# Kernel tuning notes

Hardware: AMD Instinct MI355X
Metric: run time of the kernel (lower is better)

The kernel has to match this reference:

```python
import jax, jax.numpy as jnp
import numpy as np

N, M, G = 50000, 400000, 128   # nodes, undirected edges, graphs
FN, FE, L, O = 128, 32, 128, 128
MAX_LV = 3


def setup_inputs() -> dict:
    rng = np.random.default_rng(0)
    key = jax.random.key(0)
    ks = jax.random.split(key, 12)
    # random multigraph without self-loops; directed edges interleaved so that
    # edge 2i = (u->v) and edge 2i+1 = (v->u) (reverse edge = e ^ 1)
    u = rng.integers(0, N, size=M)
    v = (u + 1 + rng.integers(0, N - 1, size=M)) % N
    src = np.empty(2 * M, dtype=np.int32)
    dst = np.empty(2 * M, dtype=np.int32)
    src[0::2], src[1::2] = u, v
    dst[0::2], dst[1::2] = v, u
    graph_ids = np.sort(rng.integers(0, G, size=N)).astype(np.int32)

    def lin(k, fan_in, fan_out):
        return jax.random.normal(k, (fan_in, fan_out), jnp.float32) / np.sqrt(fan_in)

    return {
        "node_feat": jax.random.normal(ks[0], (N, FN), jnp.float32),
        "edge_feat": jax.random.normal(ks[1], (2 * M, FE), jnp.float32),
        "w_n2l_W": lin(ks[2], FN, L), "w_n2l_b": jnp.zeros((L,), jnp.float32),
        "w_e2l_W": lin(ks[3], FE, L), "w_e2l_b": jnp.zeros((L,), jnp.float32),
        "conv_W": lin(ks[4], L, L),   "conv_b": jnp.zeros((L,), jnp.float32),
        "out_W": lin(ks[5], L, O),    "out_b": jnp.zeros((O,), jnp.float32),
        "edge_src": jnp.asarray(src),
        "edge_dst": jnp.asarray(dst),
        "graph_ids": jnp.asarray(graph_ids),
        "num_graphs": G,
    }


def _swap_reverse(msgs):
    # message of the reverse directed edge: pairs are interleaved (2i, 2i+1)
    E, D = msgs.shape
    return msgs.reshape(E // 2, 2, D)[:, ::-1, :].reshape(E, D)


def reference(node_feat, edge_feat, w_n2l_W, w_n2l_b, w_e2l_W, w_e2l_b,
              conv_W, conv_b, out_W, out_b, edge_src, edge_dst, graph_ids,
              num_graphs):
    n_nodes = node_feat.shape[0]
    # n2e_sp @ (W_n node_feat): gather source-node linear features onto edges
    input_node_linear = node_feat @ w_n2l_W + w_n2l_b          # [N, L]
    input_message = input_node_linear[edge_src]                # [E, L]
    input_message = input_message + (edge_feat @ w_e2l_W + w_e2l_b)
    cur = jax.nn.relu(input_message)                           # input_potential
    for _ in range(MAX_LV):
        # e2e_sp @ cur: sum of messages into src node, minus reverse edge
        node_agg = jax.ops.segment_sum(cur, edge_dst, num_segments=n_nodes)
        e2epool = node_agg[edge_src] - _swap_reverse(cur)      # [E, L]
        cur = jax.nn.relu(e2epool @ conv_W + conv_b + input_message)
    # e2n_sp @ cur: sum edge messages into destination nodes
    e2npool = jax.ops.segment_sum(cur, edge_dst, num_segments=n_nodes)
    hidden_msg = jax.nn.relu(e2npool)                          # [N, L]
    reluact = jax.nn.relu(hidden_msg @ out_W + out_b)          # [N, O]
    # subg_sp @ reluact: pool nodes per graph
    y = jax.ops.segment_sum(reluact, graph_ids, num_segments=num_graphs)
    return jax.nn.relu(y)                                      # [G, O]
```

## Files before the change

kernel.cpp:

```cpp
#include <hip/hip_runtime.h>
#include <hip/hip_bf16.h>
#include <stdint.h>

typedef __attribute__((ext_vector_type(8))) short short8;
typedef __attribute__((ext_vector_type(4))) float f32x4;

__device__ __forceinline__ float b2f(ushort u) {
  union { uint32_t i; float f; } v; v.i = ((uint32_t)u) << 16; return v.f;
}
__device__ __forceinline__ ushort f2b(float f) {
  union { float f; uint32_t i; } v; v.f = f;
  uint32_t x = v.i;
  uint32_t r = x + 0x7FFFu + ((x >> 16) & 1u);
  return (ushort)(r >> 16);
}
__device__ __forceinline__ uint pk2(float lo, float hi) {
  return (uint)f2b(lo) | ((uint)f2b(hi) << 16);
}
__device__ __forceinline__ float lo2f(uint v) { return b2f((ushort)(v & 0xFFFFu)); }
__device__ __forceinline__ float hi2f(uint v) { return b2f((ushort)(v >> 16)); }

__device__ __forceinline__ uint4 pkf8(float4 a, float4 b) {
  uint4 o;
  o.x = pk2(a.x, a.y); o.y = pk2(a.z, a.w);
  o.z = pk2(b.x, b.y); o.w = pk2(b.z, b.w);
  return o;
}
__device__ __forceinline__ uint sub2(uint a, uint b) {
  return pk2(lo2f(a) - lo2f(b), hi2f(a) - hi2f(b));
}
__device__ __forceinline__ uint4 sub8(uint4 a, uint4 b) {
  uint4 o; o.x = sub2(a.x,b.x); o.y = sub2(a.y,b.y); o.z = sub2(a.z,b.z); o.w = sub2(a.w,b.w); return o;
}
__device__ __forceinline__ uint relu2(uint v) {
  uint lo = (v & 0x8000u) ? 0u : (v & 0xFFFFu);
  uint hi = (v & 0x80000000u) ? 0u : (v & 0xFFFF0000u);
  return lo | hi;
}
__device__ __forceinline__ uint4 relu8(uint4 v) {
  uint4 o; o.x = relu2(v.x); o.y = relu2(v.y); o.z = relu2(v.z); o.w = relu2(v.w); return o;
}

__global__ void zero_ints(int* __restrict__ p, int n) {
  int i = blockIdx.x * blockDim.x + threadIdx.x;
  if (i < n) p[i] = 0;
}

__global__ void prep_weights(const float* __restrict__ wn, const float* __restrict__ we,
                             const float* __restrict__ cw, const float* __restrict__ ow,
                             const float* __restrict__ cb, const float* __restrict__ be,
                             ushort* __restrict__ wnT, ushort* __restrict__ weT,
                             ushort* __restrict__ cweT, ushort* __restrict__ owT,
                             float* __restrict__ cbe) {
  int i = blockIdx.x * blockDim.x + threadIdx.x;
  if (i < 16384) {
    int n = i >> 7, k = i & 127; wnT[n*128+k] = f2b(wn[k*128+n]);
  } else if (i < 32768) {
    int j = i - 16384; int n = j >> 7, k = j & 127; owT[n*128+k] = f2b(ow[k*128+n]);
  } else if (i < 53248) {
    int j = i - 32768;
    int n = j / 160, k = j % 160;
    cweT[n*160+k] = (k < 128) ? f2b(cw[k*128+n]) : f2b(we[(k-128)*128+n]);
  } else if (i < 57344) {
    int j = i - 53248; int n = j >> 5, k = j & 31; weT[n*32+k] = f2b(we[k*128+n]);
  } else if (i < 57472) {
    int j = i - 57344; cbe[j] = cb[j] + be[j];
  }
}

__global__ void count_dst(const int* __restrict__ dst, int* __restrict__ counts, int E) {
  for (int i = blockIdx.x * blockDim.x + threadIdx.x; i < E; i += gridDim.x * blockDim.x)
    atomicAdd(&counts[dst[i]], 1);
}
__global__ __launch_bounds__(1024) void scan_offsets(
    const int* __restrict__ counts, int* __restrict__ off,
    int* __restrict__ cursor, int N) {
  __shared__ int part[1024];
  int t = threadIdx.x;
  int chunk = (N + 1023) >> 10;
  int lo = t * chunk, hi = min(lo + chunk, N);
  int s = 0;
  for (int i = lo; i < hi; ++i) s += counts[i];
  part[t] = s;
  __syncthreads();
  for (int d = 1; d < 1024; d <<= 1) {
    int v = (t >= d) ? part[t - d] : 0;
    __syncthreads();
    part[t] += v;
    __syncthreads();
  }
  int run = (t > 0) ? part[t - 1] : 0;
  for (int i = lo; i < hi; ++i) {
    off[i] = run; cursor[i] = run; run += counts[i];
  }
  if (t == 1023) off[N] = part[1023];
}
__global__ void fill_csr(const int* __restrict__ dst, int* __restrict__ cursor,
                         int* __restrict__ eids, int E) {
  for (int i = blockIdx.x * blockDim.x + threadIdx.x; i < E; i += gridDim.x * blockDim.x) {
    int p = atomicAdd(&cursor[dst[i]], 1);
    eids[p] = i;
  }
}

__global__ __launch_bounds__(256) void node_linear(
    const float* __restrict__ nf, const ushort* __restrict__ wnT,
    const float* __restrict__ bn, ushort* __restrict__ inl, int N) {
  __shared__ ushort Als[64][136];
  __shared__ ushort Bls[128][136];
  int tid = threadIdx.x;
  int n0 = blockIdx.x * 64;
  {
    int row = tid >> 1, h = tid & 1;
    const uint4* gp = (const uint4*)(wnT + row*128 + h*64);
    uint4* lp = (uint4*)&Bls[row][h*64];
    #pragma unroll
    for (int i = 0; i < 8; ++i) lp[i] = gp[i];
  }
  {
    int r = tid >> 2, q = tid & 3;
    int n = n0 + r;
    uint4* lp = (uint4*)&Als[r][q*32];
    if (n < N) {
      const float4* fp = (const float4*)(nf + (size_t)n*128 + q*32);
      #pragma unroll
      for (int i = 0; i < 4; ++i) lp[i] = pkf8(fp[2*i], fp[2*i+1]);
    } else {
      uint4 z = {0,0,0,0};
      #pragma unroll
      for (int i = 0; i < 4; ++i) lp[i] = z;
    }
  }
  __syncthreads();
  int l = tid & 63, w = tid >> 6, quad = l >> 4, mr = l & 15;
  f32x4 acc[8];
  #pragma unroll
  for (int nt = 0; nt < 8; ++nt) acc[nt] = (f32x4){0.f,0.f,0.f,0.f};
  #pragma unroll
  for (int kk = 0; kk < 4; ++kk) {
    short8 a = *(const short8*)&Als[w*16 + mr][kk*32 + quad*8];
    #pragma unroll
    for (int nt = 0; nt < 8; ++nt) {
      short8 b = *(const short8*)&Bls[nt*16 + mr][kk*32 + quad*8];
      acc[nt] = __builtin_amdgcn_mfma_f32_16x16x32_bf16(a, b, acc[nt], 0, 0, 0);
    }
  }
  #pragma unroll
  for (int nt = 0; nt < 8; ++nt) {
    int col = nt*16 + mr;
    float bias = bn[col];
    #pragma unroll
    for (int rg = 0; rg < 4; ++rg) {
      int n = n0 + w*16 + quad*4 + rg;
      if (n < N) inl[(size_t)n*128 + col] = f2b(acc[nt][rg] + bias);
    }
  }
}

__global__ __launch_bounds__(256) void edge_init(
    const float* __restrict__ ef, const ushort* __restrict__ weT,
    const float* __restrict__ be, const int* __restrict__ esrc,
    const ushort* __restrict__ inl, ushort* __restrict__ cur, int E) {
  __shared__ ushort Als[64][40];
  __shared__ ushort Bls[128][40];
  int tid = threadIdx.x;
  int e0 = blockIdx.x * 64;
  {
    int row = tid >> 1, h = tid & 1;
    const uint4* gp = (const uint4*)(weT + row*32 + h*16);
    uint4* lp = (uint4*)&Bls[row][h*16];
    lp[0] = gp[0]; lp[1] = gp[1];
  }
  {
    int r = tid >> 2, q = tid & 3;
    int e = e0 + r;
    const float4* fp = (const float4*)(ef + (size_t)e*32 + q*8);
    *(uint4*)&Als[r][q*8] = pkf8(fp[0], fp[1]);
  }
  __syncthreads();
  int l = tid & 63, w = tid >> 6, quad = l >> 4, mr = l & 15;
  short8 a = *(const short8*)&Als[w*16 + mr][quad*8];
  f32x4 zero = (f32x4){0.f,0.f,0.f,0.f};
  f32x4 acc[8];
  #pragma unroll
  for (int nt = 0; nt < 8; ++nt) {
    short8 b = *(const short8*)&Bls[nt*16 + mr][quad*8];
    acc[nt] = __builtin_amdgcn_mfma_f32_16x16x32_bf16(a, b, zero, 0, 0, 0);
  }
  int sfour[4];
  #pragma unroll
  for (int rg = 0; rg < 4; ++rg) sfour[rg] = esrc[e0 + w*16 + quad*4 + rg];
  #pragma unroll
  for (int nt = 0; nt < 8; ++nt) {
    int col = nt*16 + mr;
    float bias = be[col];
    #pragma unroll
    for (int rg = 0; rg < 4; ++rg) {
      int e = e0 + w*16 + quad*4 + rg;
      float v = acc[nt][rg] + bias + b2f(inl[(size_t)sfour[rg]*128 + col]);
      cur[(size_t)e*128 + col] = f2b(fmaxf(v, 0.f));
    }
  }
}

__global__ __launch_bounds__(256) void segsum(
    const ushort* __restrict__ cur, const int* __restrict__ off,
    const int* __restrict__ eids, ushort* __restrict__ nagg, int N) {
  int w = threadIdx.x >> 6, l = threadIdx.x & 63;
  int n = blockIdx.x * 4 + w;
  if (n >= N) return;
  int i = off[n], end = off[n + 1];
  float s0 = 0.f, s1 = 0.f;
  for (; i + 4 <= end; i += 4) {
    int ea = eids[i], eb = eids[i + 1], ec = eids[i + 2], ed = eids[i + 3];
    uint va = *(const uint*)(cur + (size_t)ea*128 + 2*l);
    uint vb = *(const uint*)(cur + (size_t)eb*128 + 2*l);
    uint vc = *(const uint*)(cur + (size_t)ec*128 + 2*l);
    uint vd = *(const uint*)(cur + (size_t)ed*128 + 2*l);
    s0 += (lo2f(va) + lo2f(vb)) + (lo2f(vc) + lo2f(vd));
    s1 += (hi2f(va) + hi2f(vb)) + (hi2f(vc) + hi2f(vd));
  }
  for (; i < end; ++i) {
    int ea = eids[i];
    uint va = *(const uint*)(cur + (size_t)ea*128 + 2*l);
    s0 += lo2f(va); s1 += hi2f(va);
  }
  *(uint*)(nagg + (size_t)n*128 + 2*l) = pk2(s0, s1);
}

__global__ __launch_bounds__(256) void conv_step(
    ushort* __restrict__ cur, const ushort* __restrict__ nagg,
    const ushort* __restrict__ inl, const float* __restrict__ ef,
    const ushort* __restrict__ cweT, const float* __restrict__ cbe,
    const int* __restrict__ esrc, int E) {
  __shared__ ushort Als[64][168];
  int tid = threadIdx.x;
  int e0 = blockIdx.x * 64;
  int l = tid & 63, w = tid >> 6, quad = l >> 4, mr = l & 15;

  short8 bfrag[2][5];
  #pragma unroll
  for (int nt = 0; nt < 2; ++nt) {
    const ushort* bp = cweT + (size_t)(w*32 + nt*16 + mr) * 160;
    #pragma unroll
    for (int kk = 0; kk < 5; ++kk)
      bfrag[nt][kk] = *(const short8*)(bp + kk*32 + quad*8);
  }

  {
    int r = tid >> 2, q = tid & 3;
    int e = e0 + r;
    int s = esrc[e];
    const uint4* cp = (const uint4*)(cur + (size_t)(e ^ 1)*128 + q*32);
    const uint4* np = (const uint4*)(nagg + (size_t)s*128 + q*32);
    uint4* lp = (uint4*)&Als[r][q*32];
    #pragma unroll
    for (int i = 0; i < 4; ++i) lp[i] = sub8(np[i], cp[i]);
    const float4* fp = (const float4*)(ef + (size_t)e*32 + q*8);
    *(uint4*)&Als[r][128 + q*8] = pkf8(fp[0], fp[1]);
  }
  __syncthreads();

  #pragma unroll
  for (int m = 0; m < 4; ++m) {
    f32x4 acc0 = (f32x4){0.f,0.f,0.f,0.f};
    f32x4 acc1 = (f32x4){0.f,0.f,0.f,0.f};
    #pragma unroll
    for (int kk = 0; kk < 5; ++kk) {
      short8 a = *(const short8*)&Als[m*16 + mr][kk*32 + quad*8];
      acc0 = __builtin_amdgcn_mfma_f32_16x16x32_bf16(a, bfrag[0][kk], acc0, 0, 0, 0);
      acc1 = __builtin_amdgcn_mfma_f32_16x16x32_bf16(a, bfrag[1][kk], acc1, 0, 0, 0);
    }
    int ebase = e0 + m*16 + quad*4;
    int sfour[4];
    #pragma unroll
    for (int rg = 0; rg < 4; ++rg) sfour[rg] = esrc[ebase + rg];
    int col0 = w*32 + mr, col1 = w*32 + 16 + mr;
    float bias0 = cbe[col0], bias1 = cbe[col1];
    #pragma unroll
    for (int rg = 0; rg < 4; ++rg) {
      float v0 = acc0[rg] + bias0 + b2f(inl[(size_t)sfour[rg]*128 + col0]);
      float v1 = acc1[rg] + bias1 + b2f(inl[(size_t)sfour[rg]*128 + col1]);
      cur[(size_t)(ebase + rg)*128 + col0] = f2b(fmaxf(v0, 0.f));
      cur[(size_t)(ebase + rg)*128 + col1] = f2b(fmaxf(v1, 0.f));
    }
  }
}

__global__ __launch_bounds__(256) void out_linear(
    const ushort* __restrict__ nagg, const ushort* __restrict__ owT,
    const float* __restrict__ ob, ushort* __restrict__ ract, int N) {
  __shared__ ushort Als[64][136];
  __shared__ ushort Bls[128][136];
  int tid = threadIdx.x;
  int n0 = blockIdx.x * 64;
  {
    int row = tid >> 1, h = tid & 1;
    const uint4* gp = (const uint4*)(owT + row*128 + h*64);
    uint4* lp = (uint4*)&Bls[row][h*64];
    #pragma unroll
    for (int i = 0; i < 8; ++i) lp[i] = gp[i];
  }
  {
    int r = tid >> 2, q = tid & 3;
    int n = n0 + r;
    uint4* lp = (uint4*)&Als[r][q*32];
    if (n < N) {
      const uint4* gp = (const uint4*)(nagg + (size_t)n*128 + q*32);
      #pragma unroll
      for (int i = 0; i < 4; ++i) lp[i] = relu8(gp[i]);
    } else {
      uint4 z = {0,0,0,0};
      #pragma unroll
      for (int i = 0; i < 4; ++i) lp[i] = z;
    }
  }
  __syncthreads();
  int l = tid & 63, w = tid >> 6, quad = l >> 4, mr = l & 15;
  f32x4 acc[8];
  #pragma unroll
  for (int nt = 0; nt < 8; ++nt) acc[nt] = (f32x4){0.f,0.f,0.f,0.f};
  #pragma unroll
  for (int kk = 0; kk < 4; ++kk) {
    short8 a = *(const short8*)&Als[w*16 + mr][kk*32 + quad*8];
    #pragma unroll
    for (int nt = 0; nt < 8; ++nt) {
      short8 b = *(const short8*)&Bls[nt*16 + mr][kk*32 + quad*8];
      acc[nt] = __builtin_amdgcn_mfma_f32_16x16x32_bf16(a, b, acc[nt], 0, 0, 0);
    }
  }
  #pragma unroll
  for (int nt = 0; nt < 8; ++nt) {
    int col = nt*16 + mr;
    float bias = ob[col];
    #pragma unroll
    for (int rg = 0; rg < 4; ++rg) {
      int n = n0 + w*16 + quad*4 + rg;
      if (n < N) ract[(size_t)n*128 + col] = f2b(fmaxf(acc[nt][rg] + bias, 0.f));
    }
  }
}

__global__ void graph_offsets(const int* __restrict__ gids, int* __restrict__ goff,
                              int N, int G) {
  int i = blockIdx.x * blockDim.x + threadIdx.x;
  if (i > N) return;
  int pg = (i == 0) ? -1 : gids[i - 1];
  int cg = (i == N) ? G : gids[i];
  for (int g = pg + 1; g <= cg; ++g) goff[g] = i;
}

__global__ __launch_bounds__(256) void graph_pool(
    const ushort* __restrict__ ract, const int* __restrict__ goff,
    float* __restrict__ out, int G) {
  __shared__ float red0[256];
  __shared__ float red1[256];
  int g = blockIdx.x;
  int t = threadIdx.x;
  int c2 = t & 63, rp = t >> 6;
  int beg = goff[g], end = goff[g + 1];
  float s0 = 0.f, s1 = 0.f;
  for (int n = beg + rp; n < end; n += 4) {
    uint v = *(const uint*)(ract + (size_t)n*128 + 2*c2);
    s0 += lo2f(v); s1 += hi2f(v);
  }
  red0[t] = s0; red1[t] = s1;
  __syncthreads();
  if (rp == 0) {
    float v0 = red0[c2] + red0[c2 + 64] + red0[c2 + 128] + red0[c2 + 192];
    float v1 = red1[c2] + red1[c2 + 64] + red1[c2 + 128] + red1[c2 + 192];
    float2 o; o.x = fmaxf(v0, 0.f); o.y = fmaxf(v1, 0.f);
    *(float2*)(out + (size_t)g*128 + 2*c2) = o;
  }
}

extern "C" void kernel_launch(void* const* d_in, const int* in_sizes, int n_in,
                              void* d_out, int out_size, void* d_ws, size_t ws_size,
                              hipStream_t stream) {
  const float* node_feat = (const float*)d_in[0];
  const float* edge_feat = (const float*)d_in[1];
  const float* wn = (const float*)d_in[2];
  const float* bn = (const float*)d_in[3];
  const float* we = (const float*)d_in[4];
  const float* be = (const float*)d_in[5];
  const float* cw = (const float*)d_in[6];
  const float* cb = (const float*)d_in[7];
  const float* ow = (const float*)d_in[8];
  const float* ob = (const float*)d_in[9];
  const int* esrc = (const int*)d_in[10];
  const int* edst = (const int*)d_in[11];
  const int* gids = (const int*)d_in[12];
  int N = in_sizes[0] / 128;
  int E = in_sizes[10];
  int G = out_size / 128;
  float* out = (float*)d_out;

  char* p = (char*)d_ws;
  auto alloc = [&](size_t bytes) {
    char* r = p;
    p += (bytes + 255) & ~(size_t)255;
    return r;
  };
  ushort* cur     = (ushort*)alloc((size_t)E * 128 * 2);
  ushort* inl     = (ushort*)alloc((size_t)N * 128 * 2);
  ushort* nagg    = (ushort*)alloc((size_t)N * 128 * 2);
  int*    eids    = (int*)   alloc((size_t)E * 4);
  int*    counts  = (int*)   alloc((size_t)N * 4);
  int*    off     = (int*)   alloc((size_t)(N + 1) * 4);
  int*    cursor  = (int*)   alloc((size_t)N * 4);
  int*    goff    = (int*)   alloc((size_t)(G + 1) * 4);
  ushort* wnT     = (ushort*)alloc(128 * 128 * 2);
  ushort* weT     = (ushort*)alloc(128 * 32 * 2);
  ushort* cweT    = (ushort*)alloc(128 * 160 * 2);
  ushort* owT     = (ushort*)alloc(128 * 128 * 2);
  float*  cbe     = (float*) alloc(128 * 4);
  ushort* ract    = inl;
  (void)ws_size; (void)n_in;

  zero_ints<<<(N + 255) / 256, 256, 0, stream>>>(counts, N);
  prep_weights<<<225, 256, 0, stream>>>(wn, we, cw, ow, cb, be, wnT, weT, cweT, owT, cbe);
  count_dst<<<1024, 256, 0, stream>>>(edst, counts, E);
  scan_offsets<<<1, 1024, 0, stream>>>(counts, off, cursor, N);
  fill_csr<<<1024, 256, 0, stream>>>(edst, cursor, eids, E);

  node_linear<<<(N + 63) / 64, 256, 0, stream>>>(node_feat, wnT, bn, inl, N);
  edge_init<<<E / 64, 256, 0, stream>>>(edge_feat, weT, be, esrc, inl, cur, E);

  for (int it = 0; it < 3; ++it) {
    segsum<<<(N + 3) / 4, 256, 0, stream>>>(cur, off, eids, nagg, N);
    conv_step<<<E / 64, 256, 0, stream>>>(cur, nagg, inl, edge_feat, cweT, cbe, esrc, E);
  }
  segsum<<<(N + 3) / 4, 256, 0, stream>>>(cur, off, eids, nagg, N);
  out_linear<<<(N + 63) / 64, 256, 0, stream>>>(nagg, owT, ob, ract, N);
  graph_offsets<<<(N + 256) / 256, 256, 0, stream>>>(gids, goff, N, G);
  graph_pool<<<G, 256, 0, stream>>>(ract, goff, out, G);
}
```

Measured before the change: 1.334 ms.

## Stage MFMA outputs in LDS for coalesced 16-byte epilogue stores and gathers

```diff
diff --git a/kernel.cpp b/kernel.cpp
--- a/kernel.cpp
+++ b/kernel.cpp
@@ -31,6 +31,13 @@
 }
 __device__ __forceinline__ uint4 sub8(uint4 a, uint4 b) {
   uint4 o; o.x = sub2(a.x,b.x); o.y = sub2(a.y,b.y); o.z = sub2(a.z,b.z); o.w = sub2(a.w,b.w); return o;
+}
+__device__ __forceinline__ uint addrelu2(uint a, uint b) {
+  return pk2(fmaxf(lo2f(a) + lo2f(b), 0.f), fmaxf(hi2f(a) + hi2f(b), 0.f));
+}
+__device__ __forceinline__ uint4 addrelu8(uint4 a, uint4 b) {
+  uint4 o; o.x = addrelu2(a.x,b.x); o.y = addrelu2(a.y,b.y);
+  o.z = addrelu2(a.z,b.z); o.w = addrelu2(a.w,b.w); return o;
 }
 __device__ __forceinline__ uint relu2(uint v) {
   uint lo = (v & 0x8000u) ? 0u : (v & 0xFFFFu);
@@ -162,44 +169,48 @@
     const float* __restrict__ be, const int* __restrict__ esrc,
     const ushort* __restrict__ inl, ushort* __restrict__ cur, int E) {
   __shared__ ushort Als[64][40];
-  __shared__ ushort Bls[128][40];
+  __shared__ ushort Cls[64][136];
   int tid = threadIdx.x;
   int e0 = blockIdx.x * 64;
-  {
-    int row = tid >> 1, h = tid & 1;
-    const uint4* gp = (const uint4*)(weT + row*32 + h*16);
-    uint4* lp = (uint4*)&Bls[row][h*16];
-    lp[0] = gp[0]; lp[1] = gp[1];
-  }
-  {
-    int r = tid >> 2, q = tid & 3;
+  int l = tid & 63, w = tid >> 6, quad = l >> 4, mr = l & 15;
+  int r = tid >> 2, q = tid & 3;
+
+  short8 bfrag[2];
+  #pragma unroll
+  for (int nt = 0; nt < 2; ++nt)
+    bfrag[nt] = *(const short8*)(weT + (size_t)(w*32 + nt*16 + mr)*32 + quad*8);
+
+  {
+    const float4* fp = (const float4*)(ef + (size_t)(e0 + r)*32 + q*8);
+    *(uint4*)&Als[r][q*8] = pkf8(fp[0], fp[1]);
+  }
+  __syncthreads();
+
+  int col0 = w*32 + mr, col1 = w*32 + 16 + mr;
+  float bias0 = be[col0], bias1 = be[col1];
+  #pragma unroll
+  for (int m = 0; m < 4; ++m) {
+    short8 a = *(const short8*)&Als[m*16 + mr][quad*8];
+    f32x4 zero = (f32x4){0.f,0.f,0.f,0.f};
+    f32x4 acc0 = __builtin_amdgcn_mfma_f32_16x16x32_bf16(a, bfrag[0], zero, 0, 0, 0);
+    f32x4 acc1 = __builtin_amdgcn_mfma_f32_16x16x32_bf16(a, bfrag[1], zero, 0, 0, 0);
+    #pragma unroll
+    for (int rg = 0; rg < 4; ++rg) {
+      int row = m*16 + quad*4 + rg;
+      Cls[row][col0] = f2b(acc0[rg] + bias0);
+      Cls[row][col1] = f2b(acc1[rg] + bias1);
+    }
+  }
+  __syncthreads();
+
+  {
     int e = e0 + r;
-    const float4* fp = (const float4*)(ef + (size_t)e*32 + q*8);
-    *(uint4*)&Als[r][q*8] = pkf8(fp[0], fp[1]);
-  }
-  __syncthreads();
-  int l = tid & 63, w = tid >> 6, quad = l >> 4, mr = l & 15;
-  short8 a = *(const short8*)&Als[w*16 + mr][quad*8];
-  f32x4 zero = (f32x4){0.f,0.f,0.f,0.f};
-  f32x4 acc[8];
-  #pragma unroll
-  for (int nt = 0; nt < 8; ++nt) {
-    short8 b = *(const short8*)&Bls[nt*16 + mr][quad*8];
-    acc[nt] = __builtin_amdgcn_mfma_f32_16x16x32_bf16(a, b, zero, 0, 0, 0);
-  }
-  int sfour[4];
-  #pragma unroll
-  for (int rg = 0; rg < 4; ++rg) sfour[rg] = esrc[e0 + w*16 + quad*4 + rg];
-  #pragma unroll
-  for (int nt = 0; nt < 8; ++nt) {
-    int col = nt*16 + mr;
-    float bias = be[col];
-    #pragma unroll
-    for (int rg = 0; rg < 4; ++rg) {
-      int e = e0 + w*16 + quad*4 + rg;
-      float v = acc[nt][rg] + bias + b2f(inl[(size_t)sfour[rg]*128 + col]);
-      cur[(size_t)e*128 + col] = f2b(fmaxf(v, 0.f));
-    }
+    int s = esrc[e];
+    const uint4* cl = (const uint4*)&Cls[r][q*32];
+    const uint4* ip = (const uint4*)(inl + (size_t)s*128 + q*32);
+    uint4* op = (uint4*)(cur + (size_t)e*128 + q*32);
+    #pragma unroll
+    for (int i = 0; i < 4; ++i) op[i] = addrelu8(cl[i], ip[i]);
   }
 }
 
@@ -211,14 +222,14 @@
   if (n >= N) return;
   int i = off[n], end = off[n + 1];
   float s0 = 0.f, s1 = 0.f;
-  for (; i + 4 <= end; i += 4) {
-    int ea = eids[i], eb = eids[i + 1], ec = eids[i + 2], ed = eids[i + 3];
-    uint va = *(const uint*)(cur + (size_t)ea*128 + 2*l);
-    uint vb = *(const uint*)(cur + (size_t)eb*128 + 2*l);
-    uint vc = *(const uint*)(cur + (size_t)ec*128 + 2*l);
-    uint vd = *(const uint*)(cur + (size_t)ed*128 + 2*l);
-    s0 += (lo2f(va) + lo2f(vb)) + (lo2f(vc) + lo2f(vd));
-    s1 += (hi2f(va) + hi2f(vb)) + (hi2f(vc) + hi2f(vd));
+  for (; i + 8 <= end; i += 8) {
+    int e[8]; uint v[8];
+    #pragma unroll
+    for (int j = 0; j < 8; ++j) e[j] = eids[i + j];
+    #pragma unroll
+    for (int j = 0; j < 8; ++j) v[j] = *(const uint*)(cur + (size_t)e[j]*128 + 2*l);
+    #pragma unroll
+    for (int j = 0; j < 8; ++j) { s0 += lo2f(v[j]); s1 += hi2f(v[j]); }
   }
   for (; i < end; ++i) {
     int ea = eids[i];
@@ -234,9 +245,11 @@
     const ushort* __restrict__ cweT, const float* __restrict__ cbe,
     const int* __restrict__ esrc, int E) {
   __shared__ ushort Als[64][168];
+  __shared__ ushort Cls[64][136];
   int tid = threadIdx.x;
   int e0 = blockIdx.x * 64;
   int l = tid & 63, w = tid >> 6, quad = l >> 4, mr = l & 15;
+  int r = tid >> 2, q = tid & 3;
 
   short8 bfrag[2][5];
   #pragma unroll
@@ -248,7 +261,6 @@
   }
 
   {
-    int r = tid >> 2, q = tid & 3;
     int e = e0 + r;
     int s = esrc[e];
     const uint4* cp = (const uint4*)(cur + (size_t)(e ^ 1)*128 + q*32);
@@ -261,6 +273,8 @@
   }
   __syncthreads();
 
+  int col0 = w*32 + mr, col1 = w*32 + 16 + mr;
+  float bias0 = cbe[col0], bias1 = cbe[col1];
   #pragma unroll
   for (int m = 0; m < 4; ++m) {
     f32x4 acc0 = (f32x4){0.f,0.f,0.f,0.f};
@@ -271,19 +285,23 @@
       acc0 = __builtin_amdgcn_mfma_f32_16x16x32_bf16(a, bfrag[0][kk], acc0, 0, 0, 0);
       acc1 = __builtin_amdgcn_mfma_f32_16x16x32_bf16(a, bfrag[1][kk], acc1, 0, 0, 0);
     }
-    int ebase = e0 + m*16 + quad*4;
-    int sfour[4];
-    #pragma unroll
-    for (int rg = 0; rg < 4; ++rg) sfour[rg] = esrc[ebase + rg];
-    int col0 = w*32 + mr, col1 = w*32 + 16 + mr;
-    float bias0 = cbe[col0], bias1 = cbe[col1];
     #pragma unroll
     for (int rg = 0; rg < 4; ++rg) {
-      float v0 = acc0[rg] + bias0 + b2f(inl[(size_t)sfour[rg]*128 + col0]);
-      float v1 = acc1[rg] + bias1 + b2f(inl[(size_t)sfour[rg]*128 + col1]);
-      cur[(size_t)(ebase + rg)*128 + col0] = f2b(fmaxf(v0, 0.f));
-      cur[(size_t)(ebase + rg)*128 + col1] = f2b(fmaxf(v1, 0.f));
-    }
+      int row = m*16 + quad*4 + rg;
+      Cls[row][col0] = f2b(acc0[rg] + bias0);
+      Cls[row][col1] = f2b(acc1[rg] + bias1);
+    }
+  }
+  __syncthreads();
+
+  {
+    int e = e0 + r;
+    int s = esrc[e];
+    const uint4* cl = (const uint4*)&Cls[r][q*32];
+    const uint4* ip = (const uint4*)(inl + (size_t)s*128 + q*32);
+    uint4* op = (uint4*)(cur + (size_t)e*128 + q*32);
+    #pragma unroll
+    for (int i = 0; i < 4; ++i) op[i] = addrelu8(cl[i], ip[i]);
   }
 }
 
```

Measured after the change: 1.179 ms. 1.13x faster.
